# Kernel optimization log

Hardware: AMD Instinct MI355X
Metric: run time of the kernel (lower is better)

Reference implementation:

```python
import jax, jax.numpy as jnp
import numpy as np

NEURAL_DIM = 512
N_UNITS = 512
N_DAYS = 24
N_CLASSES = 41
N_LAYERS = 5
PATCH = 14
STRIDE = 4
MEMORY_SIZE = 256
IN0 = NEURAL_DIM * PATCH  # 7168, layer-0 input after patch concat


def _expm(M):
    """Matrix exponential via scaling-and-squaring + Taylor (float64 numpy)."""
    nrm = np.linalg.norm(M, 1)
    s = max(0, int(np.ceil(np.log2(nrm))) + 4) if nrm > 0 else 0
    Ms = M / (2.0 ** s)
    n = M.shape[0]
    E = np.eye(n)
    term = np.eye(n)
    for k in range(1, 25):
        term = term @ Ms / k
        E = E + term
    for _ in range(s):
        E = E @ E
    return E


def _lmu_AB(m_size):
    # NOTE: the torch cell calls _compute_A_B(memory_size, B.shape[0]), so the
    # effective theta used for discretization is memory_size itself.
    theta = float(m_size)
    q = np.arange(m_size, dtype=np.float64)
    R = ((2.0 * q + 1.0) / theta).reshape(-1, 1)
    i, j = np.meshgrid(q, q, indexing='ij')
    A = R * np.where(i < j, -1.0, (-1.0) ** (i - j + 1))
    Bc = R * ((-1.0) ** q).reshape(-1, 1)
    # zero-order hold discretization with dt=1: expm([[A,B],[0,0]])
    aug = np.zeros((m_size + 1, m_size + 1))
    aug[:m_size, :m_size] = A
    aug[:m_size, m_size:] = Bc
    E = _expm(aug)
    return (jnp.asarray(E[:m_size, :m_size], dtype=jnp.float32),
            jnp.asarray(E[:m_size, m_size:], dtype=jnp.float32))


A_MAT, B_MAT = _lmu_AB(MEMORY_SIZE)  # [M,M], [M,1]


def setup_inputs() -> dict:
    key = jax.random.key(0)
    ks = jax.random.split(key, 20)

    def rn(k, shape, scale):
        return jax.random.normal(k, shape, dtype=jnp.float32) * scale

    inp = {
        'x': jax.random.normal(ks[0], (32, 1024, NEURAL_DIM), dtype=jnp.float32),
        'day_idx': jax.random.randint(ks[1], (32,), 0, N_DAYS),
        # day-specific input layers (init: identity + zero bias; perturb slightly)
        'day_W': jnp.broadcast_to(jnp.eye(NEURAL_DIM, dtype=jnp.float32), (N_DAYS, NEURAL_DIM, NEURAL_DIM)) + rn(ks[2], (N_DAYS, NEURAL_DIM, NEURAL_DIM), 0.01),
        'day_b': rn(ks[3], (N_DAYS, 1, NEURAL_DIM), 0.01),
        # layer 0 (input 7168)
        'e_x0': rn(ks[4], (1, IN0), 1.0 / np.sqrt(IN0)),
        'W_x0': rn(ks[5], (N_UNITS, IN0), np.sqrt(2.0 / (IN0 + N_UNITS))),
        # layers 1..4 (input 512)
        'e_xr': rn(ks[6], (N_LAYERS - 1, 1, N_UNITS), 1.0 / np.sqrt(N_UNITS)),
        'W_xr': rn(ks[7], (N_LAYERS - 1, N_UNITS, N_UNITS), np.sqrt(1.0 / N_UNITS)),
        # shared-shape per-layer params (stacked over 5 layers)
        'e_h': rn(ks[8], (N_LAYERS, 1, N_UNITS), 1.0 / np.sqrt(N_UNITS)),
        'e_m': rn(ks[9], (N_LAYERS, 1, MEMORY_SIZE), 0.02),
        'W_h': rn(ks[10], (N_LAYERS, N_UNITS, N_UNITS), np.sqrt(1.0 / N_UNITS)),
        'W_m': rn(ks[11], (N_LAYERS, N_UNITS, MEMORY_SIZE), np.sqrt(2.0 / (MEMORY_SIZE + N_UNITS))),
        'h0': rn(ks[12], (N_LAYERS, 1, N_UNITS), 0.05),
        'm0': rn(ks[13], (N_LAYERS, 1, MEMORY_SIZE), 0.05),
        'out_W': rn(ks[14], (N_CLASSES, N_UNITS), np.sqrt(2.0 / (N_UNITS + N_CLASSES))),
        'out_b': jnp.zeros((N_CLASSES,), dtype=jnp.float32),
    }
    return inp


def _run_lmu_layer(seq, e_x, W_x, e_h, e_m, W_h, W_m, h_init, m_init):
    """seq: [B,T,in] -> [B,T,H] LMU recurrence."""
    # precompute input projections (the only big GEMMs) outside the scan
    xWx = jnp.einsum('bti,hi->bth', seq, W_x)   # [B,T,H]
    xex = jnp.einsum('bti,oi->bto', seq, e_x)   # [B,T,1]

    def step(carry, inp):
        h, m = carry
        xw, xe = inp
        u = xe + h @ e_h.T + m @ e_m.T          # [B,1]
        m = m @ A_MAT.T + u @ B_MAT.T           # [B,M]
        h = jnp.tanh(xw + h @ W_h.T + m @ W_m.T)
        return (h, m), h

    (_, _), hs = jax.lax.scan(step, (h_init, m_init),
                              (jnp.swapaxes(xWx, 0, 1), jnp.swapaxes(xex, 0, 1)))
    return jnp.swapaxes(hs, 0, 1)  # [B,T,H]


def reference(x, day_idx, day_W, day_b, e_x0, W_x0, e_xr, W_xr,
              e_h, e_m, W_h, W_m, h0, m0, out_W, out_b):
    B = x.shape[0]
    # day-specific linear + softsign
    h = jnp.einsum('btd,bdk->btk', x, day_W[day_idx]) + day_b[day_idx]
    h = h / (1.0 + jnp.abs(h))  # Softsign
    # patch concat: unfold time dim with window=PATCH, stride=STRIDE
    T = h.shape[1]
    Tp = (T - PATCH) // STRIDE + 1
    idx = jnp.arange(Tp)[:, None] * STRIDE + jnp.arange(PATCH)[None, :]
    h = h[:, idx, :].reshape(B, Tp, PATCH * NEURAL_DIM)  # [B,Tp,7168]

    bc = lambda v, d: jnp.broadcast_to(v, (B, d))
    seq = _run_lmu_layer(h, e_x0, W_x0, e_h[0], e_m[0], W_h[0], W_m[0],
                         bc(h0[0], N_UNITS), bc(m0[0], MEMORY_SIZE))
    for i in range(1, N_LAYERS):
        seq = _run_lmu_layer(seq, e_xr[i - 1], W_xr[i - 1], e_h[i], e_m[i],
                             W_h[i], W_m[i], bc(h0[i], N_UNITS), bc(m0[i], MEMORY_SIZE))
    logits = seq @ out_W.T + out_b  # [B,Tp,n_classes]
    return logits
```

## Files before the change

### kernel.cpp

```cpp
#include <hip/hip_runtime.h>
#include <hip/hip_fp16.h>

typedef _Float16 f16;
typedef _Float16 f16x8 __attribute__((ext_vector_type(8)));
typedef _Float16 f16x4 __attribute__((ext_vector_type(4)));
typedef float f32x4 __attribute__((ext_vector_type(4)));
typedef int int4v __attribute__((ext_vector_type(4)));

#define DI static __device__ __forceinline__

constexpr int N2 = 257 * 257;
#define LSTRIDE ((size_t)254 * 32 * 768)

DI f32x4 mfma16(f16x8 a, f16x8 b, f32x4 c) {
  return __builtin_amdgcn_mfma_f32_16x16x32_f16(a, b, c, 0, 0, 0);
}
DI f16x8 ldg8(const f16* p) { return *reinterpret_cast<const f16x8*>(p); }
DI f16x8 cvt8(const float* s) {
  f16x8 v;
#pragma unroll
  for (int j = 0; j < 8; ++j) v[j] = (f16)s[j];
  return v;
}
DI double invfact(int k) {
  double f = 1.0;
  for (int i = 2; i <= k; ++i) f *= (double)i;
  return 1.0 / f;
}

DI void st_d_sc1(double* p, double v) {
  asm volatile("global_store_dwordx2 %0, %1, off sc1" :: "v"(p), "v"(v) : "memory");
}
DI void st_f_sc1(float* p, float v) {
  asm volatile("global_store_dword %0, %1, off sc1" :: "v"(p), "v"(v) : "memory");
}
DI void st_h_sc1(f16* p, f16 v) {
  asm volatile("global_store_short %0, %1, off sc1" :: "v"(p), "v"(v) : "memory");
}
DI void st_b_sc1(unsigned char* p, int v) {
  asm volatile("global_store_byte %0, %1, off sc1" :: "v"(p), "v"(v) : "memory");
}
DI void st8_sc1(f16* p, f16x4 v) {
  asm volatile("global_store_dwordx2 %0, %1, off sc1\n\ts_waitcnt vmcnt(0)"
               :: "v"(p), "v"(v) : "memory");
}
DI int ld_llc(const int* p) {
  return __hip_atomic_load(p, __ATOMIC_RELAXED, __HIP_MEMORY_SCOPE_AGENT);
}
DI void add_llc(int* p) {
  __hip_atomic_fetch_add(p, 1, __ATOMIC_RELAXED, __HIP_MEMORY_SCOPE_AGENT);
}
DI void drain_vm() { asm volatile("s_waitcnt vmcnt(0)" ::: "memory"); }
DI void membar() {
  __builtin_amdgcn_sched_barrier(0);
  asm volatile("" ::: "memory");
}
DI bool all_one(int4v a) {
  return a.x == 0x01010101 && a.y == 0x01010101 && a.z == 0x01010101 && a.w == 0x01010101;
}
DI void poll_one(const int* p) {
  for (int it = 0; it < (1 << 14); ++it) {
    int4v a;
    asm volatile("global_load_dwordx4 %0, %1, off sc1\n\ts_waitcnt vmcnt(0)"
                 : "=v"(a) : "v"(p) : "memory");
    if (all_one(a)) return;
    __builtin_amdgcn_s_sleep(1);
  }
}
DI void poll_two(const int* pa, const int* pb) {
  for (int it = 0; it < (1 << 14); ++it) {
    int4v a, b;
    asm volatile(
        "global_load_dwordx4 %0, %2, off sc1\n\t"
        "global_load_dwordx4 %1, %3, off sc1\n\t"
        "s_waitcnt vmcnt(0)"
        : "=&v"(a), "=&v"(b) : "v"(pa), "v"(pb) : "memory");
    if (all_one(a) && all_one(b)) return;
    __builtin_amdgcn_s_sleep(1);
  }
}
DI float tanh_fast(float x) {
  x = fminf(9.f, fmaxf(-9.f, x));
  float e = __expf(2.f * x);
  return __fdividef(e - 1.f, e + 1.f);
}

DI void gridbar_nf(int* bar, int nwg) {
  drain_vm();
  __syncthreads();
  if (threadIdx.x == 0) {
    int g = ld_llc(bar + 1);
    int old = __hip_atomic_fetch_add(bar, 1, __ATOMIC_RELAXED, __HIP_MEMORY_SCOPE_AGENT);
    if (old == nwg - 1) {
      __hip_atomic_store(bar, 0, __ATOMIC_RELAXED, __HIP_MEMORY_SCOPE_AGENT);
      add_llc(bar + 1);
    } else {
      for (int it = 0; it < (1 << 14) && ld_llc(bar + 1) == g; ++it)
        __builtin_amdgcn_s_sleep(1);
    }
  }
  __syncthreads();
}

DI void mm257(double* __restrict__ D, const double* __restrict__ A, const double* __restrict__ Bm,
              int fj, const double* __restrict__ T1, const double* __restrict__ T2,
              const double* __restrict__ T3, int gtid, int nth) {
  double c0 = 0, c1 = 0, c2 = 0, c3 = 0;
  if (fj >= 0) {
    c0 = invfact(4 * fj); c1 = invfact(4 * fj + 1);
    c2 = invfact(4 * fj + 2); c3 = invfact(4 * fj + 3);
  }
  for (int e = gtid; e < N2; e += nth) {
    int i = e / 257, j = e - i * 257;
    const double* ar = A + (size_t)i * 257;
    const double* bc = Bm + j;
    double s0 = 0, s1 = 0, s2 = 0, s3 = 0;
    for (int k = 0; k < 256; k += 4) {
      s0 = fma(ar[k], bc[(size_t)k * 257], s0);
      s1 = fma(ar[k + 1], bc[(size_t)(k + 1) * 257], s1);
      s2 = fma(ar[k + 2], bc[(size_t)(k + 2) * 257], s2);
      s3 = fma(ar[k + 3], bc[(size_t)(k + 3) * 257], s3);
    }
    double s = ((s0 + s1) + (s2 + s3)) + ar[256] * bc[(size_t)256 * 257];
    if (fj >= 0) s += c0 * ((i == j) ? 1.0 : 0.0) + c1 * T1[e] + c2 * T2[e] + c3 * T3[e];
    st_d_sc1(D + e, s);
  }
}

__global__ __launch_bounds__(256) void k_setup(
    const float* __restrict__ dayW, const float* __restrict__ ex0, const float* __restrict__ Wx0,
    const float* __restrict__ exr, const float* __restrict__ Wxr,
    const float* __restrict__ eh, const float* __restrict__ em,
    const float* __restrict__ Wh, const float* __restrict__ Wm, const float* __restrict__ outW,
    double* __restrict__ X, float* __restrict__ w1f, float* __restrict__ AWt,
    float* __restrict__ btf, f16* __restrict__ gbuf, f16* __restrict__ wxcat,
    f16* __restrict__ outw, f16* __restrict__ dayWt, int* __restrict__ bar) {
  const int gtid = blockIdx.x * 256 + threadIdx.x;
  const int nth = 128 * 256;
  double* Ms = X;
  double* M2 = X + N2;
  double* M3 = X + 2 * N2;
  double* M4 = X + 3 * N2;
  double* H = X + 4 * N2;
  double* S = X + 11 * N2;

  for (int e = gtid; e < N2; e += nth) {
    int i = e / 257, j = e - i * 257;
    double v = 0.0;
    if (i < 256) {
      double R = (2.0 * i + 1.0) / 256.0;
      if (j < 256) v = R * ((i < j) ? -1.0 : (((i - j) & 1) ? 1.0 : -1.0));
      else v = R * ((i & 1) ? -1.0 : 1.0);
    }
    st_d_sc1(Ms + e, v / 64.0);
  }
  for (int e = gtid; e < 576 * 896; e += nth) {
    int n = e / 896, kc = (e - n * 896) * 8;
    f16x8 v;
    if (n < 512) v = cvt8(Wx0 + (size_t)n * 7168 + kc);
    else if (n == 512) v = cvt8(ex0 + kc);
    else {
#pragma unroll
      for (int j = 0; j < 8; ++j) v[j] = (f16)0.f;
    }
    *reinterpret_cast<f16x8*>(wxcat + (size_t)n * 7168 + kc) = v;
  }
  for (int e = gtid; e < 48 * 64; e += nth) {
    int n = e / 64, kc = (e - n * 64) * 8;
    f16x8 v;
    if (n < 41) v = cvt8(outW + (size_t)n * 512 + kc);
    else {
#pragma unroll
      for (int j = 0; j < 8; ++j) v[j] = (f16)0.f;
    }
    *reinterpret_cast<f16x8*>(outw + (size_t)n * 512 + kc) = v;
  }
  {
    __shared__ float tile[64][65];
    for (int tt = blockIdx.x; tt < 24 * 64; tt += 128) {
      int D = tt >> 6; int r = tt & 63; int kb = (r >> 3) * 64; int nb = (r & 7) * 64;
      __syncthreads();
      for (int q = 0; q < 16; ++q) {
        int idx = threadIdx.x + q * 256; int kk = idx >> 6; int nn = idx & 63;
        tile[kk][nn] = dayW[(size_t)D * 262144 + (size_t)(kb + kk) * 512 + nb + nn];
      }
      __syncthreads();
      for (int q = 0; q < 2; ++q) {
        int cidx = threadIdx.x + q * 256; int nn = cidx >> 3; int kc = (cidx & 7) * 8;
        f16x8 v;
#pragma unroll
        for (int jj = 0; jj < 8; ++jj) v[jj] = (f16)tile[kc + jj][nn];
        *reinterpret_cast<f16x8*>(dayWt + (size_t)D * 262144 + (size_t)(nb + nn) * 512 + kb + kc) = v;
      }
    }
    __syncthreads();
  }
  gridbar_nf(bar, 128);

  mm257(M2, Ms, Ms, -1, Ms, Ms, Ms, gtid, nth); gridbar_nf(bar, 128);
  mm257(M3, M2, Ms, -1, Ms, Ms, Ms, gtid, nth); gridbar_nf(bar, 128);
  mm257(M4, M2, M2, -1, Ms, Ms, Ms, gtid, nth);
  for (int e = gtid; e < N2; e += nth) {
    int i = e / 257, j = e - i * 257;
    st_d_sc1(H + e, (i == j) ? invfact(24) : 0.0);
  }
  gridbar_nf(bar, 128);
  for (int k = 0; k < 6; ++k) {
    mm257(H + (size_t)(k + 1) * N2, H + (size_t)k * N2, M4, 5 - k, Ms, M2, M3, gtid, nth);
    gridbar_nf(bar, 128);
  }
  {
    const double* Ssrc = H + (size_t)6 * N2;
    for (int k = 0; k < 6; ++k) {
      mm257(S + (size_t)k * N2, Ssrc, Ssrc, -1, Ms, Ms, Ms, gtid, nth);
      gridbar_nf(bar, 128);
      Ssrc = S + (size_t)k * N2;
    }
  }
  const double* E = S + (size_t)5 * N2;

  for (int e = gtid; e < 256; e += nth) st_f_sc1(btf + e, (float)E[(size_t)e * 257 + 256]);
  for (int e = gtid; e < 5 * 512; e += nth) {
    int l = e / 512, n = e - l * 512;
    const float* wm = Wm + ((size_t)l * 512 + n) * 256;
    float s = 0.f;
    for (int j = 0; j < 256; ++j) s += (float)E[(size_t)j * 257 + 256] * wm[j];
    st_f_sc1(w1f + e, s);
  }
  for (int e = gtid; e < 5 * 512 * 256; e += nth) {
    int l = e / (512 * 256); int r = e - l * 512 * 256; int n = r >> 8; int i = r & 255;
    const double* Ec = E + i;
    const float* wm = Wm + ((size_t)l * 512 + n) * 256;
    float s0 = 0, s1 = 0, s2 = 0, s3 = 0;
    for (int j = 0; j < 256; j += 4) {
      s0 += (float)Ec[(size_t)j * 257] * wm[j];
      s1 += (float)Ec[(size_t)(j + 1) * 257] * wm[j + 1];
      s2 += (float)Ec[(size_t)(j + 2) * 257] * wm[j + 2];
      s3 += (float)Ec[(size_t)(j + 3) * 257] * wm[j + 3];
    }
    st_f_sc1(AWt + e, (s0 + s1) + (s2 + s3));
  }
  gridbar_nf(bar, 128);

  for (int e = gtid; e < 5 * 768 * 160; e += nth) {
    int l = e / (768 * 160); int r = e - l * 768 * 160; int n = r / 160; int k = (r - n * 160) * 8;
    if (l == 0 && k >= 768) continue;
    f16x8 v;
    if (n < 512) {
      float w1n = w1f[l * 512 + n];
      if (k < 512) {
        const float* a = Wh + ((size_t)l * 512 + n) * 512 + k;
        const float* b = eh + (size_t)l * 512 + k;
#pragma unroll
        for (int jj = 0; jj < 8; ++jj) v[jj] = (f16)(a[jj] + b[jj] * w1n);
      } else if (k < 768) {
        int i = k - 512;
        const float* a = AWt + ((size_t)l * 512 + n) * 256 + i;
        const float* b = em + (size_t)l * 256 + i;
#pragma unroll
        for (int jj = 0; jj < 8; ++jj) v[jj] = (f16)(a[jj] + b[jj] * w1n);
      } else {
        int d = k - 768;
        const float* a = Wxr + ((size_t)(l - 1) * 512 + n) * 512 + d;
        const float* b = exr + (size_t)(l - 1) * 512 + d;
#pragma unroll
        for (int jj = 0; jj < 8; ++jj) v[jj] = (f16)(a[jj] + b[jj] * w1n);
      }
    } else {
      int jm = n - 512;
      float btn = btf[jm];
      if (k < 512) {
        const float* b = eh + (size_t)l * 512 + k;
#pragma unroll
        for (int jj = 0; jj < 8; ++jj) v[jj] = (f16)(b[jj] * btn);
      } else if (k < 768) {
        int i = k - 512;
        const double* a = E + (size_t)jm * 257 + i;
        const float* b = em + (size_t)l * 256 + i;
#pragma unroll
        for (int jj = 0; jj < 8; ++jj) v[jj] = (f16)((float)a[jj] + b[jj] * btn);
      } else {
        int d = k - 768;
        const float* b = exr + (size_t)(l - 1) * 512 + d;
#pragma unroll
        for (int jj = 0; jj < 8; ++jj) v[jj] = (f16)(b[jj] * btn);
      }
    }
    *reinterpret_cast<f16x8*>(gbuf + ((size_t)l * 768 + n) * 1280 + k) = v;
  }
}

__global__ __launch_bounds__(256) void k_day(const float* __restrict__ x,
    const int* __restrict__ dayIdx, const float* __restrict__ dayb,
    const f16* __restrict__ dayWt, f16* __restrict__ h1) {
  __shared__ f16 As[64][40];
  __shared__ f16 Bs[256][40];
  const int bid = blockIdx.x;
  const int b = bid >> 5; const int r = bid & 31;
  const int t0 = (r >> 1) * 64; const int n0 = (r & 1) * 256;
  const int D = dayIdx[b];
  const int tid = threadIdx.x, lane = tid & 63, w = tid >> 6, q4 = lane >> 4;
  const float* xb = x + ((size_t)b * 1024 + t0) * 512;
  const f16* Wt = dayWt + (size_t)D * 262144 + (size_t)n0 * 512;
  f32x4 acc[16];
#pragma unroll
  for (int i = 0; i < 16; ++i) acc[i] = (f32x4){0.f, 0.f, 0.f, 0.f};
  for (int kt = 0; kt < 16; ++kt) {
    const int k0 = kt * 32;
    __syncthreads();
    { int row = tid >> 2, c8 = (tid & 3) * 8;
      *reinterpret_cast<f16x8*>(&As[row][c8]) = cvt8(xb + (size_t)row * 512 + k0 + c8); }
    for (int q = 0; q < 4; ++q) {
      int idx = tid + q * 256; int row = idx >> 2; int c8 = (idx & 3) * 8;
      *reinterpret_cast<f16x8*>(&Bs[row][c8]) = ldg8(Wt + (size_t)row * 512 + k0 + c8);
    }
    __syncthreads();
    f16x8 a = *reinterpret_cast<const f16x8*>(&As[w * 16 + (lane & 15)][q4 * 8]);
#pragma unroll
    for (int nt2 = 0; nt2 < 16; ++nt2) {
      f16x8 bb = *reinterpret_cast<const f16x8*>(&Bs[nt2 * 16 + (lane & 15)][q4 * 8]);
      acc[nt2] = mfma16(a, bb, acc[nt2]);
    }
  }
#pragma unroll
  for (int nt2 = 0; nt2 < 16; ++nt2) {
    int n = n0 + nt2 * 16 + (lane & 15);
    float db = dayb[(size_t)D * 512 + n];
#pragma unroll
    for (int i = 0; i < 4; ++i) {
      int t = t0 + w * 16 + q4 * 4 + i;
      float v = acc[nt2][i] + db;
      v = v / (1.f + fabsf(v));
      h1[((size_t)b * 1024 + t) * 512 + n] = (f16)v;
    }
  }
}

__global__ __launch_bounds__(256) void k_xw0(const f16* __restrict__ h1,
    const f16* __restrict__ wxcat, float* __restrict__ xw0) {
  __shared__ f16 As[128][40];
  __shared__ f16 Bs[96][40];
  const int bid = blockIdx.x;
  const int mt = bid / 6; const int nb = bid - mt * 6;
  const int m0 = mt * 128; const int n0 = nb * 96;
  const int tid = threadIdx.x, lane = tid & 63, w = tid >> 6, q4 = lane >> 4;
  f32x4 acc[2][6];
#pragma unroll
  for (int a = 0; a < 2; ++a)
#pragma unroll
    for (int b = 0; b < 6; ++b) acc[a][b] = (f32x4){0.f, 0.f, 0.f, 0.f};
  for (int kt = 0; kt < 224; ++kt) {
    const int k0 = kt * 32; const int p = k0 >> 9; const int kd = k0 & 511;
    __syncthreads();
    for (int q = 0; q < 2; ++q) {
      int idx = tid + q * 256; int row = idx >> 2; int c8 = (idx & 3) * 8;
      int m = m0 + row; int b = m >> 8; int tp = m & 255; if (tp > 252) tp = 252;
      *reinterpret_cast<f16x8*>(&As[row][c8]) =
          ldg8(h1 + ((size_t)b * 1024 + (size_t)tp * 4 + p) * 512 + kd + c8);
    }
    for (int q = 0; q < 2; ++q) {
      int idx = tid + q * 256;
      if (idx < 384) {
        int row = idx >> 2; int c8 = (idx & 3) * 8;
        *reinterpret_cast<f16x8*>(&Bs[row][c8]) =
            ldg8(wxcat + (size_t)(n0 + row) * 7168 + k0 + c8);
      }
    }
    __syncthreads();
#pragma unroll
    for (int mb = 0; mb < 2; ++mb) {
      f16x8 a = *reinterpret_cast<const f16x8*>(&As[w * 32 + mb * 16 + (lane & 15)][q4 * 8]);
#pragma unroll
      for (int nt2 = 0; nt2 < 6; ++nt2) {
        f16x8 bb = *reinterpret_cast<const f16x8*>(&Bs[nt2 * 16 + (lane & 15)][q4 * 8]);
        acc[mb][nt2] = mfma16(a, bb, acc[mb][nt2]);
      }
    }
  }
#pragma unroll
  for (int mb = 0; mb < 2; ++mb)
#pragma unroll
    for (int nt2 = 0; nt2 < 6; ++nt2)
#pragma unroll
      for (int i = 0; i < 4; ++i) {
        int m = m0 + w * 32 + mb * 16 + q4 * 4 + i;
        int n = n0 + nt2 * 16 + (lane & 15);
        xw0[(size_t)m * 576 + n] = acc[mb][nt2][i];
      }
}

template <int KK>
DI void rec_run(int l, int c, int tid, const f16* __restrict__ gbuf, f16* __restrict__ sbuf,
                const float* __restrict__ xw0, const float* __restrict__ w1f,
                const float* __restrict__ btf, const float* __restrict__ h0,
                const float* __restrict__ m0, unsigned char* done, f16* bflds, f16* smtile) {
  const int lane = tid & 63, w = tid >> 6;
  const int mb = w / 3, nt = w % 3;
  const int nbase = c * 48 + nt * 16;
  const int ncol = nbase + (lane & 15);
  const int q4 = lane >> 4;

  for (int r = tid; r < 32 * 48; r += 384) {
    int row = r / 48; int col = c * 48 + (r - row * 48);
    float v = (col < 512) ? h0[(size_t)l * 512 + col] : m0[(size_t)l * 256 + col - 512];
    st_h_sc1(sbuf + (size_t)l * LSTRIDE + (size_t)row * 768 + col, (f16)v);
  }

  const f16* gb = gbuf + ((size_t)l * 768 + ncol) * 1280 + (size_t)q4 * 8;
  constexpr int NREG = (KK > 32) ? 32 : KK;
  f16x8 bf[NREG];
#pragma unroll
  for (int kk = 0; kk < NREG; ++kk) bf[kk] = ldg8(gb + (size_t)kk * 32);
  if (KK == 40) {
#pragma unroll
    for (int kk = 32; kk < 40; ++kk) {
      f16x8 v = ldg8(gb + (size_t)kk * 32);
      *reinterpret_cast<f16x8*>(bflds + ((size_t)(w * 8 + (kk - 32)) * 64 + lane) * 8) = v;
    }
  }
  float w1n = 0.f, btn = 0.f;
  if (KK == 24) {
    if (ncol < 512) w1n = w1f[ncol];
    else btn = btf[ncol - 512];
  }
  drain_vm();
  __syncthreads();
  if (tid == 0) st_b_sc1(done + (size_t)(l * 254) * 16 + c, 1);

  for (int t = 0; t < 253; ++t) {
    float xadd[4];
    if (KK == 24) {
#pragma unroll
      for (int i = 0; i < 4; ++i) {
        const int brow = mb * 16 + q4 * 4 + i;
        const float* xr = xw0 + ((size_t)brow * 256 + t) * 576;
        float xe = xr[512];
        xadd[i] = (ncol < 512) ? (xr[ncol] + xe * w1n) : (xe * btn);
      }
    }
    if (tid == 0) {
      const int* own = (const int*)(done + (size_t)(l * 254 + t) * 16);
      if (l > 0) poll_two(own, (const int*)(done + (size_t)((l - 1) * 254 + t + 1) * 16));
      else poll_one(own);
    }
    __builtin_amdgcn_s_barrier();
    membar();

    const int arow = mb * 16 + (lane & 15);
    const f16* s0 = sbuf + (size_t)l * LSTRIDE + ((size_t)t * 32 + arow) * 768 + (size_t)q4 * 8;
    f32x4 acc = {0.f, 0.f, 0.f, 0.f};
#pragma unroll
    for (int kk = 0; kk < 24; ++kk) acc = mfma16(ldg8(s0 + (size_t)kk * 32), bf[kk < NREG ? kk : 0], acc);
    if (KK == 40) {
      const f16* s1 = sbuf + (size_t)(l - 1) * LSTRIDE + ((size_t)(t + 1) * 32 + arow) * 768 + (size_t)q4 * 8;
#pragma unroll
      for (int kk = 24; kk < 32; ++kk) acc = mfma16(ldg8(s1 + (size_t)(kk - 24) * 32), bf[kk < NREG ? kk : 0], acc);
#pragma unroll
      for (int kk = 32; kk < 40; ++kk) {
        f16x8 bb = *reinterpret_cast<const f16x8*>(bflds + ((size_t)(w * 8 + (kk - 32)) * 64 + lane) * 8);
        acc = mfma16(ldg8(s1 + (size_t)(kk - 24) * 32), bb, acc);
      }
    }

    const int scol = nt * 16 + (lane & 15);
#pragma unroll
    for (int i = 0; i < 4; ++i) {
      float v = acc[i];
      if (KK == 24) v += xadd[i];
      if (ncol < 512) v = tanh_fast(v);
      smtile[(mb * 16 + q4 * 4 + i) * 48 + scol] = (f16)v;
    }
    __syncthreads();
    {
      int row = tid / 12; int c4 = (tid - row * 12) * 4;
      f16x4 v4 = *reinterpret_cast<const f16x4*>(smtile + row * 48 + c4);
      f16* dst = sbuf + (size_t)l * LSTRIDE + ((size_t)(t + 1) * 32 + row) * 768 + c * 48 + c4;
      st8_sc1(dst, v4);
    }
    __builtin_amdgcn_s_barrier();
    if (tid == 0) st_b_sc1(done + (size_t)(l * 254 + t + 1) * 16 + c, 1);
  }
}

__global__ __launch_bounds__(384, 2) void k_rec(const f16* __restrict__ gbuf, f16* __restrict__ sbuf,
    const float* __restrict__ xw0, const float* __restrict__ w1f,
    const float* __restrict__ btf, const float* __restrict__ h0,
    const float* __restrict__ m0, unsigned char* __restrict__ done) {
  __shared__ f16 bflds[6 * 8 * 64 * 8];
  __shared__ f16 smtile[32 * 48];
  const int l = blockIdx.x & 7;
  if (l >= 5) return;
  const int c = blockIdx.x >> 3;
  if (l == 0)
    rec_run<24>(0, c, threadIdx.x, gbuf, sbuf, xw0, w1f, btf, h0, m0, done, bflds, smtile);
  else
    rec_run<40>(l, c, threadIdx.x, gbuf, sbuf, xw0, w1f, btf, h0, m0, done, bflds, smtile);
}

__global__ __launch_bounds__(256) void k_out(const f16* __restrict__ sbuf4,
    const f16* __restrict__ outw, const float* __restrict__ outb, float* __restrict__ out) {
  const int bid = blockIdx.x; const int b = bid >> 2; const int tp0 = (bid & 3) * 64;
  const int tid = threadIdx.x, lane = tid & 63, w = tid >> 6, q4 = lane >> 4;
  f32x4 acc[3];
#pragma unroll
  for (int i = 0; i < 3; ++i) acc[i] = (f32x4){0.f, 0.f, 0.f, 0.f};
  int tq = tp0 + w * 16 + (lane & 15) + 1;
  const int tau = tq > 253 ? 253 : tq;
  const f16* arow = sbuf4 + ((size_t)tau * 32 + b) * 768 + (size_t)q4 * 8;
#pragma unroll
  for (int kk = 0; kk < 16; ++kk) {
    f16x8 a = ldg8(arow + (size_t)kk * 32);
#pragma unroll
    for (int nt2 = 0; nt2 < 3; ++nt2) {
      f16x8 bb = ldg8(outw + (size_t)(nt2 * 16 + (lane & 15)) * 512 + kk * 32 + q4 * 8);
      acc[nt2] = mfma16(a, bb, acc[nt2]);
    }
  }
#pragma unroll
  for (int nt2 = 0; nt2 < 3; ++nt2) {
    int cc = nt2 * 16 + (lane & 15);
    if (cc < 41) {
      float ob = outb[cc];
#pragma unroll
      for (int i = 0; i < 4; ++i) {
        int tp = tp0 + w * 16 + q4 * 4 + i;
        if (tp < 253) out[((size_t)b * 253 + tp) * 41 + cc] = acc[nt2][i] + ob;
      }
    }
  }
}

extern "C" void kernel_launch(void* const* d_in, const int* in_sizes, int n_in,
                              void* d_out, int out_size, void* d_ws, size_t ws_size,
                              hipStream_t stream) {
  const float* x      = (const float*)d_in[0];
  const int*   dayIdx = (const int*)d_in[1];
  const float* day_W  = (const float*)d_in[2];
  const float* day_b  = (const float*)d_in[3];
  const float* e_x0   = (const float*)d_in[4];
  const float* W_x0   = (const float*)d_in[5];
  const float* e_xr   = (const float*)d_in[6];
  const float* W_xr   = (const float*)d_in[7];
  const float* e_h    = (const float*)d_in[8];
  const float* e_m    = (const float*)d_in[9];
  const float* W_h    = (const float*)d_in[10];
  const float* W_m    = (const float*)d_in[11];
  const float* h0     = (const float*)d_in[12];
  const float* m0     = (const float*)d_in[13];
  const float* out_W  = (const float*)d_in[14];
  const float* out_b  = (const float*)d_in[15];
  float* outp = (float*)d_out;

  char* w = (char*)d_ws;
  size_t o = 0;
  auto al = [&](size_t n) { void* p = w + o; o = (o + n + 255) & ~(size_t)255; return p; };

  int*   flags = (int*)  al(32768);
  f16*   gbuf  = (f16*)  al((size_t)5 * 768 * 1280 * 2);
  f16*   outw  = (f16*)  al((size_t)48 * 512 * 2);
  float* xw0   = (float*)al((size_t)8192 * 576 * 4);
  float* w1f   = (float*)al((size_t)5 * 512 * 4);
  float* btf   = (float*)al(256 * 4);

  const size_t XB    = ((size_t)17 * N2 * 8 + 255) & ~(size_t)255;
  const size_t AWTB  = ((size_t)5 * 512 * 256 * 4 + 255) & ~(size_t)255;
  const size_t DAYB  = ((size_t)24 * 512 * 512 * 2 + 255) & ~(size_t)255;
  const size_t WXB   = ((size_t)576 * 7168 * 2 + 255) & ~(size_t)255;
  const size_t H1B   = ((size_t)32 * 1024 * 512 * 2 + 255) & ~(size_t)255;
  const size_t SBUFB = (size_t)5 * LSTRIDE * 2;
  size_t ovb = XB + AWTB + DAYB + WXB + H1B;
  if (SBUFB > ovb) ovb = SBUFB;
  char* ov = (char*)al(ovb);
  double* X     = (double*)ov;
  float*  AWt   = (float*)(ov + XB);
  f16*    dayWt = (f16*)(ov + XB + AWTB);
  f16*    wxcat = (f16*)(ov + XB + AWTB + DAYB);
  f16*    h1    = (f16*)(ov + XB + AWTB + DAYB + WXB);
  f16*    sbuf  = (f16*)ov;

  if (o > ws_size) return;
  (void)in_sizes; (void)n_in; (void)out_size;

  hipMemsetAsync(flags, 0, 32768, stream);
  k_setup<<<128, 256, 0, stream>>>(day_W, e_x0, W_x0, e_xr, W_xr, e_h, e_m, W_h, W_m,
                                   out_W, X, w1f, AWt, btf, gbuf, wxcat, outw, dayWt,
                                   flags + 6144);
  k_day<<<1024, 256, 0, stream>>>(x, dayIdx, day_b, dayWt, h1);
  k_xw0<<<384, 256, 0, stream>>>(h1, wxcat, xw0);
  k_rec<<<128, 384, 0, stream>>>(gbuf, sbuf, xw0, w1f, btf, h0, m0, (unsigned char*)flags);
  k_out<<<128, 256, 0, stream>>>(sbuf + (size_t)4 * LSTRIDE, outw, out_b, outp);
}
```

Before: 4.101 ms.

## Replace done-flag polling with sentinel-filled state buffer polling in recurrence

The recurrent kernel no longer uses per-step done flags with block barriers and single-thread polling. Instead the state buffer is pre-filled with a 0x7f sentinel, and each wave spins on its own operand loads until no sentinel remains. Results are then written straight from registers with lane shuffles and paired dword stores, dropping the LDS staging tile and the two block barriers per step. This targets the per-timestep synchronisation latency of the serial recurrence. In exchange it adds a large memset of the whole state buffer and assumes no valid fp16 pair ever equals the sentinel pattern.

```diff
diff --git a/kernel.cpp b/kernel.cpp
--- a/kernel.cpp
+++ b/kernel.cpp
@@ -3,7 +3,6 @@
 
 typedef _Float16 f16;
 typedef _Float16 f16x8 __attribute__((ext_vector_type(8)));
-typedef _Float16 f16x4 __attribute__((ext_vector_type(4)));
 typedef float f32x4 __attribute__((ext_vector_type(4)));
 typedef int int4v __attribute__((ext_vector_type(4)));
 
@@ -11,6 +10,7 @@
 
 constexpr int N2 = 257 * 257;
 #define LSTRIDE ((size_t)254 * 32 * 768)
+#define SENT 0x7f7f7f7f
 
 DI f32x4 mfma16(f16x8 a, f16x8 b, f32x4 c) {
   return __builtin_amdgcn_mfma_f32_16x16x32_f16(a, b, c, 0, 0, 0);
@@ -34,15 +34,14 @@
 DI void st_f_sc1(float* p, float v) {
   asm volatile("global_store_dword %0, %1, off sc1" :: "v"(p), "v"(v) : "memory");
 }
-DI void st_h_sc1(f16* p, f16 v) {
-  asm volatile("global_store_short %0, %1, off sc1" :: "v"(p), "v"(v) : "memory");
-}
-DI void st_b_sc1(unsigned char* p, int v) {
-  asm volatile("global_store_byte %0, %1, off sc1" :: "v"(p), "v"(v) : "memory");
-}
-DI void st8_sc1(f16* p, f16x4 v) {
-  asm volatile("global_store_dwordx2 %0, %1, off sc1\n\ts_waitcnt vmcnt(0)"
-               :: "v"(p), "v"(v) : "memory");
+DI void st_dw_sc1(f16* p, int v) {
+  asm volatile("global_store_dword %0, %1, off sc1" :: "v"(p), "v"(v) : "memory");
+}
+DI void st_dw2_sc1(f16* p, int v0, int v1) {
+  asm volatile(
+      "global_store_dword %2, %0, off sc1\n\t"
+      "global_store_dword %2, %1, off offset:1536 sc1"
+      :: "v"(v0), "v"(v1), "v"(p) : "memory");
 }
 DI int ld_llc(const int* p) {
   return __hip_atomic_load(p, __ATOMIC_RELAXED, __HIP_MEMORY_SCOPE_AGENT);
@@ -51,33 +50,27 @@
   __hip_atomic_fetch_add(p, 1, __ATOMIC_RELAXED, __HIP_MEMORY_SCOPE_AGENT);
 }
 DI void drain_vm() { asm volatile("s_waitcnt vmcnt(0)" ::: "memory"); }
-DI void membar() {
+DI void wait_vm0() {
+  asm volatile("s_waitcnt vmcnt(0)" ::: "memory");
   __builtin_amdgcn_sched_barrier(0);
-  asm volatile("" ::: "memory");
-}
-DI bool all_one(int4v a) {
-  return a.x == 0x01010101 && a.y == 0x01010101 && a.z == 0x01010101 && a.w == 0x01010101;
-}
-DI void poll_one(const int* p) {
-  for (int it = 0; it < (1 << 14); ++it) {
-    int4v a;
-    asm volatile("global_load_dwordx4 %0, %1, off sc1\n\ts_waitcnt vmcnt(0)"
-                 : "=v"(a) : "v"(p) : "memory");
-    if (all_one(a)) return;
-    __builtin_amdgcn_s_sleep(1);
-  }
-}
-DI void poll_two(const int* pa, const int* pb) {
-  for (int it = 0; it < (1 << 14); ++it) {
-    int4v a, b;
-    asm volatile(
-        "global_load_dwordx4 %0, %2, off sc1\n\t"
-        "global_load_dwordx4 %1, %3, off sc1\n\t"
-        "s_waitcnt vmcnt(0)"
-        : "=&v"(a), "=&v"(b) : "v"(pa), "v"(pb) : "memory");
-    if (all_one(a) && all_one(b)) return;
-    __builtin_amdgcn_s_sleep(1);
-  }
+}
+DI void ld8i(const f16* p, f16x8* o) {
+  asm volatile(
+      "global_load_dwordx4 %0, %8, off sc1\n\t"
+      "global_load_dwordx4 %1, %8, off offset:64 sc1\n\t"
+      "global_load_dwordx4 %2, %8, off offset:128 sc1\n\t"
+      "global_load_dwordx4 %3, %8, off offset:192 sc1\n\t"
+      "global_load_dwordx4 %4, %8, off offset:256 sc1\n\t"
+      "global_load_dwordx4 %5, %8, off offset:320 sc1\n\t"
+      "global_load_dwordx4 %6, %8, off offset:384 sc1\n\t"
+      "global_load_dwordx4 %7, %8, off offset:448 sc1"
+      : "=&v"(o[0]), "=&v"(o[1]), "=&v"(o[2]), "=&v"(o[3]),
+        "=&v"(o[4]), "=&v"(o[5]), "=&v"(o[6]), "=&v"(o[7])
+      : "v"(p) : "memory");
+}
+DI bool okf(f16x8 f) {
+  int4v u = __builtin_bit_cast(int4v, f);
+  return (u.x != (int)SENT) & (u.y != (int)SENT) & (u.z != (int)SENT) & (u.w != (int)SENT);
 }
 DI float tanh_fast(float x) {
   x = fminf(9.f, fmaxf(-9.f, x));
@@ -393,17 +386,20 @@
 DI void rec_run(int l, int c, int tid, const f16* __restrict__ gbuf, f16* __restrict__ sbuf,
                 const float* __restrict__ xw0, const float* __restrict__ w1f,
                 const float* __restrict__ btf, const float* __restrict__ h0,
-                const float* __restrict__ m0, unsigned char* done, f16* bflds, f16* smtile) {
+                const float* __restrict__ m0, f16* bflds) {
   const int lane = tid & 63, w = tid >> 6;
   const int mb = w / 3, nt = w % 3;
   const int nbase = c * 48 + nt * 16;
   const int ncol = nbase + (lane & 15);
   const int q4 = lane >> 4;
 
-  for (int r = tid; r < 32 * 48; r += 384) {
-    int row = r / 48; int col = c * 48 + (r - row * 48);
-    float v = (col < 512) ? h0[(size_t)l * 512 + col] : m0[(size_t)l * 256 + col - 512];
-    st_h_sc1(sbuf + (size_t)l * LSTRIDE + (size_t)row * 768 + col, (f16)v);
+  for (int idx = tid; idx < 32 * 24; idx += 384) {
+    int row = idx / 24; int pr = idx - row * 24; int col = c * 48 + pr * 2;
+    float v0 = (col < 512) ? h0[(size_t)l * 512 + col] : m0[(size_t)l * 256 + col - 512];
+    float v1 = (col + 1 < 512) ? h0[(size_t)l * 512 + col + 1] : m0[(size_t)l * 256 + col + 1 - 512];
+    unsigned short a0 = __builtin_bit_cast(unsigned short, (f16)v0);
+    unsigned short a1 = __builtin_bit_cast(unsigned short, (f16)v1);
+    st_dw_sc1(sbuf + (size_t)l * LSTRIDE + (size_t)row * 768 + col, (int)a0 | ((int)a1 << 16));
   }
 
   const f16* gb = gbuf + ((size_t)l * 768 + ncol) * 1280 + (size_t)q4 * 8;
@@ -423,9 +419,10 @@
     if (ncol < 512) w1n = w1f[ncol];
     else btn = btf[ncol - 512];
   }
-  drain_vm();
-  __syncthreads();
-  if (tid == 0) st_b_sc1(done + (size_t)(l * 254) * 16 + c, 1);
+
+  const int arow = mb * 16 + (lane & 15);
+  const bool ev = (lane & 1) == 0;
+  const int cc = ncol & ~1;
 
   for (int t = 0; t < 253; ++t) {
     float xadd[4];
@@ -438,63 +435,72 @@
         xadd[i] = (ncol < 512) ? (xr[ncol] + xe * w1n) : (xe * btn);
       }
     }
-    if (tid == 0) {
-      const int* own = (const int*)(done + (size_t)(l * 254 + t) * 16);
-      if (l > 0) poll_two(own, (const int*)(done + (size_t)((l - 1) * 254 + t + 1) * 16));
-      else poll_one(own);
-    }
-    __builtin_amdgcn_s_barrier();
-    membar();
-
-    const int arow = mb * 16 + (lane & 15);
-    const f16* s0 = sbuf + (size_t)l * LSTRIDE + ((size_t)t * 32 + arow) * 768 + (size_t)q4 * 8;
+
     f32x4 acc = {0.f, 0.f, 0.f, 0.f};
-#pragma unroll
-    for (int kk = 0; kk < 24; ++kk) acc = mfma16(ldg8(s0 + (size_t)kk * 32), bf[kk < NREG ? kk : 0], acc);
+    {
+      const f16* s0 = sbuf + (size_t)l * LSTRIDE + ((size_t)t * 32 + arow) * 768 + (size_t)q4 * 8;
+      f16x8 sx[24];
+      for (int it = 0;; ++it) {
+        ld8i(s0, sx); ld8i(s0 + 256, sx + 8); ld8i(s0 + 512, sx + 16);
+        wait_vm0();
+        bool ok = true;
+#pragma unroll
+        for (int k2 = 0; k2 < 24; ++k2) ok &= okf(sx[k2]);
+        if (__all(ok) || it > (1 << 14)) break;
+      }
+#pragma unroll
+      for (int kk = 0; kk < 24; ++kk) acc = mfma16(sx[kk], bf[kk < NREG ? kk : 0], acc);
+    }
     if (KK == 40) {
       const f16* s1 = sbuf + (size_t)(l - 1) * LSTRIDE + ((size_t)(t + 1) * 32 + arow) * 768 + (size_t)q4 * 8;
-#pragma unroll
-      for (int kk = 24; kk < 32; ++kk) acc = mfma16(ldg8(s1 + (size_t)(kk - 24) * 32), bf[kk < NREG ? kk : 0], acc);
-#pragma unroll
-      for (int kk = 32; kk < 40; ++kk) {
-        f16x8 bb = *reinterpret_cast<const f16x8*>(bflds + ((size_t)(w * 8 + (kk - 32)) * 64 + lane) * 8);
-        acc = mfma16(ldg8(s1 + (size_t)(kk - 24) * 32), bb, acc);
-      }
-    }
-
-    const int scol = nt * 16 + (lane & 15);
+      f16x8 sy[16];
+      for (int it = 0;; ++it) {
+        ld8i(s1, sy); ld8i(s1 + 256, sy + 8);
+        wait_vm0();
+        bool ok = true;
+#pragma unroll
+        for (int k2 = 0; k2 < 16; ++k2) ok &= okf(sy[k2]);
+        if (__all(ok) || it > (1 << 14)) break;
+      }
+#pragma unroll
+      for (int kk = 0; kk < 8; ++kk) acc = mfma16(sy[kk], bf[24 + kk], acc);
+#pragma unroll
+      for (int r = 0; r < 8; ++r) {
+        f16x8 bb = *reinterpret_cast<const f16x8*>(bflds + ((size_t)(w * 8 + r) * 64 + lane) * 8);
+        acc = mfma16(sy[8 + r], bb, acc);
+      }
+    }
+
+    int myw[4];
 #pragma unroll
     for (int i = 0; i < 4; ++i) {
       float v = acc[i];
       if (KK == 24) v += xadd[i];
       if (ncol < 512) v = tanh_fast(v);
-      smtile[(mb * 16 + q4 * 4 + i) * 48 + scol] = (f16)v;
-    }
-    __syncthreads();
-    {
-      int row = tid / 12; int c4 = (tid - row * 12) * 4;
-      f16x4 v4 = *reinterpret_cast<const f16x4*>(smtile + row * 48 + c4);
-      f16* dst = sbuf + (size_t)l * LSTRIDE + ((size_t)(t + 1) * 32 + row) * 768 + c * 48 + c4;
-      st8_sc1(dst, v4);
-    }
-    __builtin_amdgcn_s_barrier();
-    if (tid == 0) st_b_sc1(done + (size_t)(l * 254 + t + 1) * 16 + c, 1);
+      myw[i] = (int)__builtin_bit_cast(unsigned short, (f16)v);
+    }
+    int pw0 = __shfl_xor(myw[0], 1), pw1 = __shfl_xor(myw[1], 1);
+    int pw2 = __shfl_xor(myw[2], 1), pw3 = __shfl_xor(myw[3], 1);
+    int d0 = ev ? (myw[0] | (pw0 << 16)) : (pw2 | (myw[2] << 16));
+    int d1 = ev ? (myw[1] | (pw1 << 16)) : (pw3 | (myw[3] << 16));
+    f16* db = sbuf + (size_t)l * LSTRIDE +
+              ((size_t)(t + 1) * 32 + (size_t)(mb * 16 + q4 * 4 + (ev ? 0 : 2))) * 768 + cc;
+    st_dw2_sc1(db, d0, d1);
   }
 }
 
 __global__ __launch_bounds__(384, 2) void k_rec(const f16* __restrict__ gbuf, f16* __restrict__ sbuf,
     const float* __restrict__ xw0, const float* __restrict__ w1f,
     const float* __restrict__ btf, const float* __restrict__ h0,
-    const float* __restrict__ m0, unsigned char* __restrict__ done) {
+    const float* __restrict__ m0) {
   __shared__ f16 bflds[6 * 8 * 64 * 8];
-  __shared__ f16 smtile[32 * 48];
   const int l = blockIdx.x & 7;
   if (l >= 5) return;
   const int c = blockIdx.x >> 3;
   if (l == 0)
-    rec_run<24>(0, c, threadIdx.x, gbuf, sbuf, xw0, w1f, btf, h0, m0, done, bflds, smtile);
+    rec_run<24>(0, c, threadIdx.x, gbuf, sbuf, xw0, w1f, btf, h0, m0, bflds);
   else
-    rec_run<40>(l, c, threadIdx.x, gbuf, sbuf, xw0, w1f, btf, h0, m0, done, bflds, smtile);
+    rec_run<40>(l, c, threadIdx.x, gbuf, sbuf, xw0, w1f, btf, h0, m0, bflds);
 }
 
 __global__ __launch_bounds__(256) void k_out(const f16* __restrict__ sbuf4,
@@ -555,7 +561,7 @@
   size_t o = 0;
   auto al = [&](size_t n) { void* p = w + o; o = (o + n + 255) & ~(size_t)255; return p; };
 
-  int*   flags = (int*)  al(32768);
+  int*   flags = (int*)  al(4096);
   f16*   gbuf  = (f16*)  al((size_t)5 * 768 * 1280 * 2);
   f16*   outw  = (f16*)  al((size_t)48 * 512 * 2);
   float* xw0   = (float*)al((size_t)8192 * 576 * 4);
@@ -581,12 +587,13 @@
   if (o > ws_size) return;
   (void)in_sizes; (void)n_in; (void)out_size;
 
-  hipMemsetAsync(flags, 0, 32768, stream);
+  hipMemsetAsync(flags, 0, 4096, stream);
   k_setup<<<128, 256, 0, stream>>>(day_W, e_x0, W_x0, e_xr, W_xr, e_h, e_m, W_h, W_m,
                                    out_W, X, w1f, AWt, btf, gbuf, wxcat, outw, dayWt,
-                                   flags + 6144);
+                                   flags);
   k_day<<<1024, 256, 0, stream>>>(x, dayIdx, day_b, dayWt, h1);
   k_xw0<<<384, 256, 0, stream>>>(h1, wxcat, xw0);
-  k_rec<<<128, 384, 0, stream>>>(gbuf, sbuf, xw0, w1f, btf, h0, m0, (unsigned char*)flags);
+  hipMemsetAsync(sbuf, 0x7f, SBUFB, stream);
+  k_rec<<<128, 384, 0, stream>>>(gbuf, sbuf, xw0, w1f, btf, h0, m0);
   k_out<<<128, 256, 0, stream>>>(sbuf + (size_t)4 * LSTRIDE, outw, out_b, outp);
 }
```

New measurement: 6.824 ms. 66.4% more time.

## Use XCD-local cache for recurrent flag/state exchange when layer blocks share an XCD

Applied to the files above, without the earlier changes.

At kernel start each recurrent block records which XCD it runs on; if all blocks of a layer land on the same XCD, that layer switches to a fast path. There it writes state and done flags with plain stores (L2-coherent within the XCD) and polls a local flag copy with sc0 loads. It keeps sc1 copies for the next layer and for the slow fallback. This targets the latency of going through the device-wide coherence level on every timestep handshake, at the cost of a startup rendezvous and dual stores.

```diff
diff --git a/kernel.cpp b/kernel.cpp
--- a/kernel.cpp
+++ b/kernel.cpp
@@ -11,6 +11,7 @@
 
 constexpr int N2 = 257 * 257;
 #define LSTRIDE ((size_t)254 * 32 * 768)
+#define HWREG_XCC_ID 63508
 
 DI f32x4 mfma16(f16x8 a, f16x8 b, f32x4 c) {
   return __builtin_amdgcn_mfma_f32_16x16x32_f16(a, b, c, 0, 0, 0);
@@ -37,12 +38,26 @@
 DI void st_h_sc1(f16* p, f16 v) {
   asm volatile("global_store_short %0, %1, off sc1" :: "v"(p), "v"(v) : "memory");
 }
+DI void st_b_plain(unsigned char* p, int v) {
+  asm volatile("global_store_byte %0, %1, off" :: "v"(p), "v"(v) : "memory");
+}
 DI void st_b_sc1(unsigned char* p, int v) {
   asm volatile("global_store_byte %0, %1, off sc1" :: "v"(p), "v"(v) : "memory");
 }
 DI void st8_sc1(f16* p, f16x4 v) {
   asm volatile("global_store_dwordx2 %0, %1, off sc1\n\ts_waitcnt vmcnt(0)"
                :: "v"(p), "v"(v) : "memory");
+}
+DI void st8_plain(f16* p, f16x4 v) {
+  asm volatile("global_store_dwordx2 %0, %1, off\n\ts_waitcnt vmcnt(0)"
+               :: "v"(p), "v"(v) : "memory");
+}
+DI void st8_dual(f16* p, f16x4 v) {
+  asm volatile(
+      "global_store_dwordx2 %0, %1, off\n\t"
+      "global_store_dwordx2 %0, %1, off sc1\n\t"
+      "s_waitcnt vmcnt(0)"
+      :: "v"(p), "v"(v) : "memory");
 }
 DI int ld_llc(const int* p) {
   return __hip_atomic_load(p, __ATOMIC_RELAXED, __HIP_MEMORY_SCOPE_AGENT);
@@ -55,27 +70,38 @@
   __builtin_amdgcn_sched_barrier(0);
   asm volatile("" ::: "memory");
 }
-DI bool all_one(int4v a) {
+DI bool l16ok(int4v a) {
   return a.x == 0x01010101 && a.y == 0x01010101 && a.z == 0x01010101 && a.w == 0x01010101;
 }
-DI void poll_one(const int* p) {
+template <bool HASP>
+DI void poll_fast(const int* ff, const int* fl, const int* pl) {
   for (int it = 0; it < (1 << 14); ++it) {
-    int4v a;
-    asm volatile("global_load_dwordx4 %0, %1, off sc1\n\ts_waitcnt vmcnt(0)"
-                 : "=v"(a) : "v"(p) : "memory");
-    if (all_one(a)) return;
+    int4v a, b, c;
+    asm volatile(
+        "global_load_dwordx4 %0, %3, off sc0\n\t"
+        "global_load_dwordx4 %1, %4, off sc1\n\t"
+        "global_load_dwordx4 %2, %5, off sc1\n\t"
+        "s_waitcnt vmcnt(0)"
+        : "=&v"(a), "=&v"(b), "=&v"(c)
+        : "v"(ff), "v"(fl), "v"(pl) : "memory");
+    bool own = l16ok(a) || l16ok(b);
+    bool prv = HASP ? l16ok(c) : true;
+    if (own & prv) return;
     __builtin_amdgcn_s_sleep(1);
   }
 }
-DI void poll_two(const int* pa, const int* pb) {
+template <bool HASP>
+DI void poll_slow(const int* fl, const int* pl) {
   for (int it = 0; it < (1 << 14); ++it) {
-    int4v a, b;
+    int4v b, c;
     asm volatile(
         "global_load_dwordx4 %0, %2, off sc1\n\t"
         "global_load_dwordx4 %1, %3, off sc1\n\t"
         "s_waitcnt vmcnt(0)"
-        : "=&v"(a), "=&v"(b) : "v"(pa), "v"(pb) : "memory");
-    if (all_one(a) && all_one(b)) return;
+        : "=&v"(b), "=&v"(c)
+        : "v"(fl), "v"(pl) : "memory");
+    bool prv = HASP ? l16ok(c) : true;
+    if (l16ok(b) & prv) return;
     __builtin_amdgcn_s_sleep(1);
   }
 }
@@ -389,11 +415,12 @@
       }
 }
 
-template <int KK>
+template <int KK, bool FAST>
 DI void rec_run(int l, int c, int tid, const f16* __restrict__ gbuf, f16* __restrict__ sbuf,
                 const float* __restrict__ xw0, const float* __restrict__ w1f,
                 const float* __restrict__ btf, const float* __restrict__ h0,
-                const float* __restrict__ m0, unsigned char* done, f16* bflds, f16* smtile) {
+                const float* __restrict__ m0, unsigned char* ffl, unsigned char* fll,
+                f16* bflds, f16* smtile) {
   const int lane = tid & 63, w = tid >> 6;
   const int mb = w / 3, nt = w % 3;
   const int nbase = c * 48 + nt * 16;
@@ -403,7 +430,9 @@
   for (int r = tid; r < 32 * 48; r += 384) {
     int row = r / 48; int col = c * 48 + (r - row * 48);
     float v = (col < 512) ? h0[(size_t)l * 512 + col] : m0[(size_t)l * 256 + col - 512];
-    st_h_sc1(sbuf + (size_t)l * LSTRIDE + (size_t)row * 768 + col, (f16)v);
+    f16* p = sbuf + (size_t)l * LSTRIDE + (size_t)row * 768 + col;
+    if (FAST) *p = (f16)v;
+    else st_h_sc1(p, (f16)v);
   }
 
   const f16* gb = gbuf + ((size_t)l * 768 + ncol) * 1280 + (size_t)q4 * 8;
@@ -425,7 +454,10 @@
   }
   drain_vm();
   __syncthreads();
-  if (tid == 0) st_b_sc1(done + (size_t)(l * 254) * 16 + c, 1);
+  if (tid == 0) {
+    if (FAST) st_b_plain(ffl + (size_t)(l * 254) * 16 + c, 1);
+    st_b_sc1(fll + (size_t)(l * 254) * 16 + c, 1);
+  }
 
   for (int t = 0; t < 253; ++t) {
     float xadd[4];
@@ -439,9 +471,16 @@
       }
     }
     if (tid == 0) {
-      const int* own = (const int*)(done + (size_t)(l * 254 + t) * 16);
-      if (l > 0) poll_two(own, (const int*)(done + (size_t)((l - 1) * 254 + t + 1) * 16));
-      else poll_one(own);
+      const int* ff = (const int*)(ffl + (size_t)(l * 254 + t) * 16);
+      const int* fl = (const int*)(fll + (size_t)(l * 254 + t) * 16);
+      const int* pl = (l > 0) ? (const int*)(fll + (size_t)((l - 1) * 254 + t + 1) * 16) : fl;
+      if (FAST) {
+        if (l > 0) poll_fast<true>(ff, fl, pl);
+        else poll_fast<false>(ff, fl, pl);
+      } else {
+        if (l > 0) poll_slow<true>(fl, pl);
+        else poll_slow<false>(fl, pl);
+      }
     }
     __builtin_amdgcn_s_barrier();
     membar();
@@ -475,26 +514,52 @@
       int row = tid / 12; int c4 = (tid - row * 12) * 4;
       f16x4 v4 = *reinterpret_cast<const f16x4*>(smtile + row * 48 + c4);
       f16* dst = sbuf + (size_t)l * LSTRIDE + ((size_t)(t + 1) * 32 + row) * 768 + c * 48 + c4;
-      st8_sc1(dst, v4);
+      if (!FAST) st8_sc1(dst, v4);
+      else if (l < 4) st8_dual(dst, v4);
+      else st8_plain(dst, v4);
     }
     __builtin_amdgcn_s_barrier();
-    if (tid == 0) st_b_sc1(done + (size_t)(l * 254 + t + 1) * 16 + c, 1);
+    if (tid == 0) {
+      if (FAST) st_b_plain(ffl + (size_t)(l * 254 + t + 1) * 16 + c, 1);
+      st_b_sc1(fll + (size_t)(l * 254 + t + 1) * 16 + c, 1);
+    }
   }
 }
 
 __global__ __launch_bounds__(384, 2) void k_rec(const f16* __restrict__ gbuf, f16* __restrict__ sbuf,
     const float* __restrict__ xw0, const float* __restrict__ w1f,
     const float* __restrict__ btf, const float* __restrict__ h0,
-    const float* __restrict__ m0, unsigned char* __restrict__ done) {
+    const float* __restrict__ m0, unsigned char* __restrict__ ffl,
+    unsigned char* __restrict__ fll, int* __restrict__ mask, int* __restrict__ ready) {
   __shared__ f16 bflds[6 * 8 * 64 * 8];
   __shared__ f16 smtile[32 * 48];
+  __shared__ int s_fast;
   const int l = blockIdx.x & 7;
   if (l >= 5) return;
   const int c = blockIdx.x >> 3;
-  if (l == 0)
-    rec_run<24>(0, c, threadIdx.x, gbuf, sbuf, xw0, w1f, btf, h0, m0, done, bflds, smtile);
-  else
-    rec_run<40>(l, c, threadIdx.x, gbuf, sbuf, xw0, w1f, btf, h0, m0, done, bflds, smtile);
+
+  if (threadIdx.x == 0) {
+    unsigned xcd = ((unsigned)__builtin_amdgcn_s_getreg(HWREG_XCC_ID)) & 15u;
+    __hip_atomic_fetch_or(mask + l, (int)(1u << xcd), __ATOMIC_RELAXED, __HIP_MEMORY_SCOPE_AGENT);
+    add_llc(ready);
+    int ok = 0;
+    for (int it = 0; it < (1 << 12); ++it) {
+      if (ld_llc(ready) >= 80) { ok = 1; break; }
+      __builtin_amdgcn_s_sleep(8);
+    }
+    int m = ld_llc(mask + l);
+    s_fast = ok && m && ((m & (m - 1)) == 0);
+  }
+  __syncthreads();
+  const bool fast = (s_fast != 0);
+
+  if (fast) {
+    if (l == 0) rec_run<24, true>(0, c, threadIdx.x, gbuf, sbuf, xw0, w1f, btf, h0, m0, ffl, fll, bflds, smtile);
+    else        rec_run<40, true>(l, c, threadIdx.x, gbuf, sbuf, xw0, w1f, btf, h0, m0, ffl, fll, bflds, smtile);
+  } else {
+    if (l == 0) rec_run<24, false>(0, c, threadIdx.x, gbuf, sbuf, xw0, w1f, btf, h0, m0, ffl, fll, bflds, smtile);
+    else        rec_run<40, false>(l, c, threadIdx.x, gbuf, sbuf, xw0, w1f, btf, h0, m0, ffl, fll, bflds, smtile);
+  }
 }
 
 __global__ __launch_bounds__(256) void k_out(const f16* __restrict__ sbuf4,
@@ -555,7 +620,7 @@
   size_t o = 0;
   auto al = [&](size_t n) { void* p = w + o; o = (o + n + 255) & ~(size_t)255; return p; };
 
-  int*   flags = (int*)  al(32768);
+  char*  flags = (char*) al(49152);
   f16*   gbuf  = (f16*)  al((size_t)5 * 768 * 1280 * 2);
   f16*   outw  = (f16*)  al((size_t)48 * 512 * 2);
   float* xw0   = (float*)al((size_t)8192 * 576 * 4);
@@ -581,12 +646,14 @@
   if (o > ws_size) return;
   (void)in_sizes; (void)n_in; (void)out_size;
 
-  hipMemsetAsync(flags, 0, 32768, stream);
+  hipMemsetAsync(flags, 0, 49152, stream);
   k_setup<<<128, 256, 0, stream>>>(day_W, e_x0, W_x0, e_xr, W_xr, e_h, e_m, W_h, W_m,
                                    out_W, X, w1f, AWt, btf, gbuf, wxcat, outw, dayWt,
-                                   flags + 6144);
+                                   (int*)(flags + 41216));
   k_day<<<1024, 256, 0, stream>>>(x, dayIdx, day_b, dayWt, h1);
   k_xw0<<<384, 256, 0, stream>>>(h1, wxcat, xw0);
-  k_rec<<<128, 384, 0, stream>>>(gbuf, sbuf, xw0, w1f, btf, h0, m0, (unsigned char*)flags);
+  k_rec<<<128, 384, 0, stream>>>(gbuf, sbuf, xw0, w1f, btf, h0, m0,
+                                 (unsigned char*)flags, (unsigned char*)(flags + 20480),
+                                 (int*)(flags + 40960), (int*)(flags + 40980));
   k_out<<<128, 256, 0, stream>>>(sbuf + (size_t)4 * LSTRIDE, outw, out_b, outp);
 }
```

After: 4.805 ms. +17.2%, slower.
